# Optimization experiments

Hardware: AMD Instinct MI355X
Metric: run time of the kernel (lower is better)

The kernel has to match this reference:

```python
import jax, jax.numpy as jnp
import numpy as np

D = 1024
H = 16
DK = D // H


def apply_rope(x):
    # x: [B, H, T, dk]; interleaved-pair RoPE as in the torch source
    T, dim = x.shape[-2], x.shape[-1]
    inv_freq = 1.0 / (10000.0 ** (jnp.arange(0, dim, 2, dtype=x.dtype) / dim))  # [dk/2]
    pos = jnp.arange(T, dtype=x.dtype)
    sinusoid = pos[:, None] * inv_freq[None, :]  # [T, dk/2]
    sin, cos = jnp.sin(sinusoid), jnp.cos(sinusoid)
    x1, x2 = x[..., ::2], x[..., 1::2]
    rot = jnp.stack([x1 * cos - x2 * sin, x1 * sin + x2 * cos], axis=-1)
    return rot.reshape(x.shape)


def setup_inputs() -> dict:
    key = jax.random.key(0)
    k1, k2, k3, k4, k5 = jax.random.split(key, 5)
    B, T = 2, 2048
    s = 1.0 / np.sqrt(D)
    return {
        "x": jax.random.normal(k1, (B, T, D), dtype=jnp.float32),
        "W_qkv": jax.random.normal(k2, (D, 3 * D), dtype=jnp.float32) * s,
        "b_qkv": jnp.zeros((3 * D,), dtype=jnp.float32),
        "W_out": jax.random.normal(k3, (D, D), dtype=jnp.float32) * s,
        "b_out": jnp.zeros((D,), dtype=jnp.float32),
    }


def reference(x, W_qkv, b_qkv, W_out, b_out):
    B, T, C = x.shape
    qkv = x @ W_qkv + b_qkv  # [B, T, 3D]
    qkv = qkv.reshape(B, T, 3, H, DK).transpose(2, 0, 3, 1, 4)  # [3, B, H, T, dk]
    q, k, v = qkv[0], qkv[1], qkv[2]
    q, k = apply_rope(q), apply_rope(k)
    scores = jnp.einsum("bhtd,bhsd->bhts", q, k) / jnp.sqrt(jnp.asarray(DK, x.dtype))
    causal = jnp.tril(jnp.ones((T, T), dtype=bool))
    scores = jnp.where(causal, scores, jnp.asarray(-1e9, x.dtype))
    probs = jax.nn.softmax(scores, axis=-1)
    attn = jnp.einsum("bhts,bhsd->bhtd", probs, v)  # [B, H, T, dk]
    out = attn.transpose(0, 2, 1, 3).reshape(B, T, C)  # b h t d -> b t (h d)
    return out @ W_out + b_out
```

## Files before the change

kernel.cpp:

```cpp
#include <hip/hip_runtime.h>
#include <math.h>

#define DMODEL 1024
#define NHEAD  16
#define HDK    64
#define BATCH  2
#define SEQ    2048
#define MROWS  (BATCH*SEQ)
#define NQKV   (3*DMODEL)
#define LOG2_10000 13.287712379549449f
#define INV2PI 0.15915494309189535f
#define SCALE_LOG2E 0.1803368801111137f
#define M_FIX 8.0f

typedef __attribute__((ext_vector_type(8))) short bf16x8;
typedef __attribute__((ext_vector_type(4))) short s16x4;
typedef __attribute__((ext_vector_type(4))) float f32x4;
typedef __attribute__((ext_vector_type(2))) unsigned int u32x2;

__device__ __forceinline__ short f2bf(float f) {
    union { float f; unsigned u; } v; v.f = f;
    unsigned r = v.u + 0x7fffu + ((v.u >> 16) & 1u);
    return (short)(r >> 16);
}

__device__ __forceinline__ float fast_exp2(float x) {
#if __has_builtin(__builtin_amdgcn_exp2f)
    return __builtin_amdgcn_exp2f(x);
#else
    return exp2f(x);
#endif
}

__device__ __forceinline__ void gld_lds16(const short* g, short* l) {
    __builtin_amdgcn_global_load_lds(
        (const __attribute__((address_space(1))) void*)g,
        (__attribute__((address_space(3))) void*)l, 16, 0, 0);
}

__global__ __launch_bounds__(256) void prep_kernel(
    const float* __restrict__ x, const float* __restrict__ wqkv,
    const float* __restrict__ wout,
    short* __restrict__ xb, short* __restrict__ wqkv_t, short* __restrict__ wout_t)
{
    __shared__ short tile[32][33];
    const int tid = threadIdx.x;
    if (blockIdx.x < 2048) {
        const int i = (blockIdx.x * 256 + tid) * 8;
        float4 a = *(const float4*)(x + i);
        float4 b = *(const float4*)(x + i + 4);
        bf16x8 o;
        o[0] = f2bf(a.x); o[1] = f2bf(a.y); o[2] = f2bf(a.z); o[3] = f2bf(a.w);
        o[4] = f2bf(b.x); o[5] = f2bf(b.y); o[6] = f2bf(b.z); o[7] = f2bf(b.w);
        *(bf16x8*)(xb + i) = o;
        return;
    }
    const int bx = blockIdx.x - 2048;
    int nx = bx & 127;
    const int ky = bx >> 7;
    const float* in; short* out; int N;
    if (nx < 96) { in = wqkv; out = wqkv_t; N = NQKV; }
    else         { in = wout; out = wout_t; N = DMODEL; nx -= 96; }
    const int tx = tid & 31, ty = tid >> 5;
    const int n0 = nx * 32, k0 = ky * 32;
    #pragma unroll
    for (int i = 0; i < 32; i += 8)
        tile[ty + i][tx] = f2bf(in[(size_t)(k0 + ty + i) * N + n0 + tx]);
    __syncthreads();
    #pragma unroll
    for (int i = 0; i < 32; i += 8)
        out[(size_t)(n0 + ty + i) * DMODEL + k0 + tx] = tile[tx][ty + i];
}

__global__ __launch_bounds__(256) void qkv_gemm_kernel(
    const short* __restrict__ xb, const short* __restrict__ Wt,
    const float* __restrict__ bias,
    short* __restrict__ qd, short* __restrict__ kd, short* __restrict__ vtb)
{
    __shared__ __align__(16) short As[3][128 * 32];
    __shared__ __align__(16) short Bs[3][128 * 32];
    const int tid = threadIdx.x;
    const int lane = tid & 63, wave = tid >> 6;
    const int wm = wave & 1, wn = wave >> 1;
    const int l15 = lane & 15, quad = lane >> 4;
    const int n0 = blockIdx.x * 128, m0 = blockIdx.y * 128;
    const int srow = lane >> 2, sc = lane & 3;
    const int scp = sc ^ ((srow >> 1) & 3);
    const int rdx = (l15 >> 1) & 3;

    const short* gA1 = xb + (size_t)(m0 + wave * 32 + srow) * DMODEL + scp * 8;
    const short* gA2 = gA1 + (size_t)16 * DMODEL;
    const short* gB1 = Wt + (size_t)(n0 + wave * 32 + srow) * DMODEL + scp * 8;
    const short* gB2 = gB1 + (size_t)16 * DMODEL;
    const int lofsA1 = (wave * 32) * 32;
    const int lofsA2 = (wave * 32 + 16) * 32;

    f32x4 zero = {0.f, 0.f, 0.f, 0.f};
    f32x4 acc[4][4];
    #pragma unroll
    for (int i = 0; i < 4; ++i)
        #pragma unroll
        for (int j = 0; j < 4; ++j) acc[i][j] = zero;

#define QKV_COMPUTE(CUR)                                                          \
    {                                                                             \
        bf16x8 af[4], bfr[4];                                                     \
        _Pragma("unroll")                                                         \
        for (int i = 0; i < 4; ++i)                                               \
            af[i] = *(const bf16x8*)&As[CUR][(wm * 64 + i * 16 + l15) * 32 + (quad ^ rdx) * 8]; \
        _Pragma("unroll")                                                         \
        for (int j = 0; j < 4; ++j)                                               \
            bfr[j] = *(const bf16x8*)&Bs[CUR][(wn * 64 + j * 16 + l15) * 32 + (quad ^ rdx) * 8]; \
        _Pragma("unroll")                                                         \
        for (int i = 0; i < 4; ++i)                                               \
            _Pragma("unroll")                                                     \
            for (int j = 0; j < 4; ++j)                                           \
                acc[i][j] = __builtin_amdgcn_mfma_f32_16x16x32_bf16(af[i], bfr[j], acc[i][j], 0, 0, 0); \
    }

    gld_lds16(gA1, &As[0][lofsA1]);
    gld_lds16(gA2, &As[0][lofsA2]);
    gld_lds16(gB1, &Bs[0][lofsA1]);
    gld_lds16(gB2, &Bs[0][lofsA2]);
    gld_lds16(gA1 + 32, &As[1][lofsA1]);
    gld_lds16(gA2 + 32, &As[1][lofsA2]);
    gld_lds16(gB1 + 32, &Bs[1][lofsA1]);
    gld_lds16(gB2 + 32, &Bs[1][lofsA2]);

    int cur = 0, nx = 2;
    #pragma unroll 3
    for (int k = 0; k < 30; ++k) {
        const int kn = (k + 2) * 32;
        gld_lds16(gA1 + kn, &As[nx][lofsA1]);
        gld_lds16(gA2 + kn, &As[nx][lofsA2]);
        gld_lds16(gB1 + kn, &Bs[nx][lofsA1]);
        gld_lds16(gB2 + kn, &Bs[nx][lofsA2]);
        asm volatile("s_waitcnt vmcnt(8)\n\ts_barrier" ::: "memory");
        QKV_COMPUTE(cur);
        asm volatile("s_barrier" ::: "memory");
        cur = (cur == 2) ? 0 : cur + 1;
        nx  = (nx == 2) ? 0 : nx + 1;
    }
    asm volatile("s_waitcnt vmcnt(4)\n\ts_barrier" ::: "memory");
    QKV_COMPUTE(cur);
    cur = (cur == 2) ? 0 : cur + 1;
    asm volatile("s_waitcnt vmcnt(0)\n\ts_barrier" ::: "memory");
    QKV_COMPUTE(cur);
#undef QKV_COMPUTE

    const int which = n0 >> 10;
    float biasv[4], invf[4];
    int hh[4], dd[4];
    #pragma unroll
    for (int j = 0; j < 4; ++j) {
        const int n = n0 + wn * 64 + j * 16 + l15;
        biasv[j] = bias[n];
        hh[j] = (n & 1023) >> 6;
        dd[j] = n & 63;
        invf[j] = INV2PI * exp2f(-((float)(dd[j] & ~1) / 64.f) * LOG2_10000);
    }
    #pragma unroll
    for (int i = 0; i < 4; ++i) {
        const int mb = m0 + wm * 64 + i * 16 + quad * 4;
        const int b = mb >> 11, tb = mb & (SEQ - 1);
        if (which < 2) {
            #pragma unroll
            for (int j = 0; j < 4; ++j) {
                #pragma unroll
                for (int r = 0; r < 4; ++r) {
                    const int t = tb + r;
                    float val = acc[i][j][r] + biasv[j];
                    const float rev = (float)t * invf[j];
                    const float fr = rev - floorf(rev);
                    const float s = __builtin_amdgcn_sinf(fr);
                    const float c = __builtin_amdgcn_cosf(fr);
                    const float partner = __shfl_xor(val, 1);
                    val = (lane & 1) ? (partner * s + val * c) : (val * c - partner * s);
                    short* dst = (which == 0) ? qd : kd;
                    dst[((size_t)(b * NHEAD + hh[j]) * SEQ + t) * HDK + dd[j]] = f2bf(val);
                }
            }
        } else {
            #pragma unroll
            for (int j = 0; j < 4; ++j) {
                s16x4 sv;
                #pragma unroll
                for (int r = 0; r < 4; ++r)
                    sv[r] = f2bf(acc[i][j][r] + biasv[j]);
                *(s16x4*)&vtb[((size_t)(b * NHEAD + hh[j]) * HDK + dd[j]) * SEQ + tb] = sv;
            }
        }
    }
}

__global__ __launch_bounds__(512) void attn_mfma_kernel(
    const short* __restrict__ qd, const short* __restrict__ kd,
    const short* __restrict__ vt, short* __restrict__ od)
{
    __shared__ __align__(16) short Ks[2][2][64 * 32];
    __shared__ __align__(16) short Vs[2][2][64 * 32];
    __shared__ __align__(16) short Ps[8][16 * 64];
    const int tid = threadIdx.x, lane = tid & 63, w = tid >> 6;
    const int l15 = lane & 15, quad = lane >> 4;
    const int par = w >> 2;
    const int ws = w & 3;
    const int id = (int)blockIdx.x;
    const int c = id & 7, g = id >> 3;
    const int qt = 31 - (g >> 2);
    const int jj = g & 3;
    const int hb = c + 8 * jj;
    const int h = hb & 15, b = hb >> 4;
    const size_t base = ((size_t)(b * NHEAD + h)) * SEQ * HDK;
    const int stid = tid & 255;
    const int hi = tid >> 8;
    const int srow = stid >> 2, sc = stid & 3;
    const int lofs = srow * 32 + (sc ^ ((srow >> 1) & 3)) * 8;
    const int rdx = (l15 >> 1) & 3;
    const int pmask = (l15 & 3) << 2;
    f32x4 zero = {0.f, 0.f, 0.f, 0.f};

    const short* kp = kd + base + (size_t)(hi * 64 + srow) * HDK + sc * 8;
    const short* vp = vt + base + (size_t)srow * SEQ + hi * 64 + sc * 8;

    const int q0 = qt * 64;
    const int trow = q0 + ws * 16 + l15;
    bf16x8 qf[2];
    {
        const short* qrow = qd + base + (size_t)trow * HDK;
        qf[0] = *(const bf16x8*)(qrow + quad * 8);
        qf[1] = *(const bf16x8*)(qrow + 32 + quad * 8);
    }
    float l_acc = 0.f;
    f32x4 o[4];
    #pragma unroll
    for (int j = 0; j < 4; ++j) o[j] = zero;

    const int nkt = qt + 1;
    const int npair = (nkt + 1) >> 1;
    short* myPs = &Ps[w][0];

    bf16x8 rk[2], rv[2];
    rk[0] = *(const bf16x8*)kp; rk[1] = *(const bf16x8*)(kp + 32);
    rv[0] = *(const bf16x8*)vp; rv[1] = *(const bf16x8*)(vp + 32);

    for (int p = 0; p < npair; ++p) {
        __syncthreads();
        *(bf16x8*)&Ks[hi][0][lofs] = rk[0];
        *(bf16x8*)&Ks[hi][1][lofs] = rk[1];
        *(bf16x8*)&Vs[hi][0][lofs] = rv[0];
        *(bf16x8*)&Vs[hi][1][lofs] = rv[1];
        __syncthreads();
        if (p + 1 < npair) {
            const int sn = (2 * p + 2) * 64;
            const short* kn = kp + (size_t)sn * HDK;
            const short* vn = vp + sn;
            rk[0] = *(const bf16x8*)kn; rk[1] = *(const bf16x8*)(kn + 32);
            rv[0] = *(const bf16x8*)vn; rv[1] = *(const bf16x8*)(vn + 32);
        }

        const int kt = 2 * p + par;
        if (kt < nkt) {
            f32x4 sacc[4];
            __builtin_amdgcn_s_setprio(1);
            #pragma unroll
            for (int j = 0; j < 4; ++j) {
                const int ro = (j * 16 + l15) * 32 + (quad ^ rdx) * 8;
                bf16x8 kf0 = *(const bf16x8*)&Ks[par][0][ro];
                bf16x8 kf1 = *(const bf16x8*)&Ks[par][1][ro];
                sacc[j] = __builtin_amdgcn_mfma_f32_16x16x32_bf16(kf0, qf[0], zero, 0, 0, 0);
                sacc[j] = __builtin_amdgcn_mfma_f32_16x16x32_bf16(kf1, qf[1], sacc[j], 0, 0, 0);
            }
            __builtin_amdgcn_s_setprio(0);
            if (kt == nkt - 1) {
                const int s0 = kt * 64;
                #pragma unroll
                for (int j = 0; j < 4; ++j) {
                    float pv[4];
                    #pragma unroll
                    for (int r = 0; r < 4; ++r) {
                        const int scol = s0 + j * 16 + quad * 4 + r;
                        const float sv = sacc[j][r] * SCALE_LOG2E - M_FIX;
                        pv[r] = (scol > trow) ? 0.f : fast_exp2(sv);
                        l_acc += pv[r];
                    }
                    unsigned pk0, pk1;
                    asm("v_cvt_pk_bf16_f32 %0, %1, %2" : "=v"(pk0) : "v"(pv[0]), "v"(pv[1]));
                    asm("v_cvt_pk_bf16_f32 %0, %1, %2" : "=v"(pk1) : "v"(pv[2]), "v"(pv[3]));
                    const int cc = (j * 4 + quad) ^ pmask;
                    u32x2 pkv = {pk0, pk1};
                    *(u32x2*)&myPs[l15 * 64 + cc * 4] = pkv;
                }
            } else {
                #pragma unroll
                for (int j = 0; j < 4; ++j) {
                    float pv[4];
                    #pragma unroll
                    for (int r = 0; r < 4; ++r) {
                        pv[r] = fast_exp2(sacc[j][r] * SCALE_LOG2E - M_FIX);
                        l_acc += pv[r];
                    }
                    unsigned pk0, pk1;
                    asm("v_cvt_pk_bf16_f32 %0, %1, %2" : "=v"(pk0) : "v"(pv[0]), "v"(pv[1]));
                    asm("v_cvt_pk_bf16_f32 %0, %1, %2" : "=v"(pk1) : "v"(pv[2]), "v"(pv[3]));
                    const int cc = (j * 4 + quad) ^ pmask;
                    u32x2 pkv = {pk0, pk1};
                    *(u32x2*)&myPs[l15 * 64 + cc * 4] = pkv;
                }
            }
            bf16x8 pf0 = *(const bf16x8*)&myPs[l15 * 64 + ((quad * 2) ^ pmask) * 4];
            bf16x8 pf1 = *(const bf16x8*)&myPs[l15 * 64 + ((8 + quad * 2) ^ pmask) * 4];
            __builtin_amdgcn_s_setprio(1);
            #pragma unroll
            for (int j = 0; j < 4; ++j) {
                const int ro = (j * 16 + l15) * 32 + (quad ^ rdx) * 8;
                bf16x8 vf0 = *(const bf16x8*)&Vs[par][0][ro];
                bf16x8 vf1 = *(const bf16x8*)&Vs[par][1][ro];
                o[j] = __builtin_amdgcn_mfma_f32_16x16x32_bf16(pf0, vf0, o[j], 0, 0, 0);
                o[j] = __builtin_amdgcn_mfma_f32_16x16x32_bf16(pf1, vf1, o[j], 0, 0, 0);
            }
            __builtin_amdgcn_s_setprio(0);
        }
    }

    float sr = l_acc;
    sr += __shfl_xor(sr, 16);
    sr += __shfl_xor(sr, 32);

    __syncthreads();
    float* ob   = (float*)&Ks[0][0][0];
    float* lbuf = (float*)&Vs[0][0][0];
    lbuf[w * 16 + l15] = sr;
    if (par == 1) {
        const int bi = (ws * 64 + lane) * 16;
        #pragma unroll
        for (int j = 0; j < 4; ++j)
            #pragma unroll
            for (int r = 0; r < 4; ++r) ob[bi + j * 4 + r] = o[j][r];
    }
    __syncthreads();
    if (par == 0) {
        const int bi = (ws * 64 + lane) * 16;
        #pragma unroll
        for (int j = 0; j < 4; ++j)
            #pragma unroll
            for (int r = 0; r < 4; ++r) o[j][r] += ob[bi + j * 4 + r];

        #pragma unroll
        for (int r = 0; r < 4; ++r) {
            const int qq = quad * 4 + r;
            const float lt = lbuf[ws * 16 + qq] + lbuf[(ws + 4) * 16 + qq];
            const float inv = 1.f / lt;
            const int t = q0 + ws * 16 + qq;
            #pragma unroll
            for (int j = 0; j < 4; ++j)
                od[((size_t)(b * SEQ + t) * NHEAD + h) * HDK + j * 16 + l15] =
                    f2bf(o[j][r] * inv);
        }
    }
}

__global__ __launch_bounds__(256) void out_gemm_kernel(
    const short* __restrict__ Ab, const short* __restrict__ Wt,
    const float* __restrict__ bias, float* __restrict__ out)
{
    __shared__ __align__(16) short As[2][128 * 32];
    __shared__ __align__(16) short Bs[2][64 * 32];
    const int tid = threadIdx.x;
    const int lane = tid & 63, wave = tid >> 6;
    const int wm = wave & 1, wn = wave >> 1;
    const int l15 = lane & 15, quad = lane >> 4;
    const int n0 = blockIdx.x * 64, m0 = blockIdx.y * 128;
    const int srow = lane >> 2, sc = lane & 3;
    const int scp = sc ^ ((srow >> 1) & 3);
    const int rdx = (l15 >> 1) & 3;

    const short* gA1 = Ab + (size_t)(m0 + wave * 32 + srow) * DMODEL + scp * 8;
    const short* gA2 = gA1 + (size_t)16 * DMODEL;
    const short* gB1 = Wt + (size_t)(n0 + wave * 16 + srow) * DMODEL + scp * 8;
    const int lofsA1 = (wave * 32) * 32;
    const int lofsA2 = (wave * 32 + 16) * 32;
    const int lofsB  = (wave * 16) * 32;

    f32x4 zero = {0.f, 0.f, 0.f, 0.f};
    f32x4 acc[4][2];
    #pragma unroll
    for (int i = 0; i < 4; ++i)
        #pragma unroll
        for (int j = 0; j < 2; ++j) acc[i][j] = zero;

    gld_lds16(gA1, &As[0][lofsA1]);
    gld_lds16(gA2, &As[0][lofsA2]);
    gld_lds16(gB1, &Bs[0][lofsB]);
    __syncthreads();

    for (int k = 0; k < DMODEL / 32; ++k) {
        const int cur = k & 1;
        if (k + 1 < DMODEL / 32) {
            const int kn = (k + 1) * 32;
            gld_lds16(gA1 + kn, &As[cur ^ 1][lofsA1]);
            gld_lds16(gA2 + kn, &As[cur ^ 1][lofsA2]);
            gld_lds16(gB1 + kn, &Bs[cur ^ 1][lofsB]);
        }
        bf16x8 af[4], bfr[2];
        #pragma unroll
        for (int i = 0; i < 4; ++i)
            af[i] = *(const bf16x8*)&As[cur][(wm * 64 + i * 16 + l15) * 32 + (quad ^ rdx) * 8];
        #pragma unroll
        for (int j = 0; j < 2; ++j)
            bfr[j] = *(const bf16x8*)&Bs[cur][(wn * 32 + j * 16 + l15) * 32 + (quad ^ rdx) * 8];
        #pragma unroll
        for (int i = 0; i < 4; ++i)
            #pragma unroll
            for (int j = 0; j < 2; ++j)
                acc[i][j] = __builtin_amdgcn_mfma_f32_16x16x32_bf16(af[i], bfr[j], acc[i][j], 0, 0, 0);
        __syncthreads();
    }

    #pragma unroll
    for (int j = 0; j < 2; ++j) {
        const int n = n0 + wn * 32 + j * 16 + l15;
        const float bv = bias[n];
        #pragma unroll
        for (int i = 0; i < 4; ++i)
            #pragma unroll
            for (int r = 0; r < 4; ++r) {
                const int m = m0 + wm * 64 + i * 16 + quad * 4 + r;
                out[(size_t)m * DMODEL + n] = acc[i][j][r] + bv;
            }
    }
}

extern "C" void kernel_launch(void* const* d_in, const int* in_sizes, int n_in,
                              void* d_out, int out_size, void* d_ws, size_t ws_size,
                              hipStream_t stream) {
    const float* x    = (const float*)d_in[0];
    const float* Wqkv = (const float*)d_in[1];
    const float* bqkv = (const float*)d_in[2];
    const float* Wout = (const float*)d_in[3];
    const float* bout = (const float*)d_in[4];
    float* out = (float*)d_out;

    short* ws = (short*)d_ws;
    short* xb     = ws;
    short* wqkv_t = xb + (size_t)4 * 1024 * 1024;
    short* wout_t = wqkv_t + (size_t)3 * 1024 * 1024;
    short* qd     = wout_t + (size_t)1024 * 1024;
    short* kd     = qd + (size_t)4 * 1024 * 1024;
    short* vtb    = kd + (size_t)4 * 1024 * 1024;
    short* attn   = vtb + (size_t)4 * 1024 * 1024;

    prep_kernel<<<2048 + 4096, 256, 0, stream>>>(x, Wqkv, Wout, xb, wqkv_t, wout_t);

    qkv_gemm_kernel<<<dim3(NQKV / 128, MROWS / 128), 256, 0, stream>>>(
        xb, wqkv_t, bqkv, qd, kd, vtb);

    attn_mfma_kernel<<<1024, 512, 0, stream>>>(qd, kd, vtb, attn);

    out_gemm_kernel<<<dim3(DMODEL / 64, MROWS / 128), 256, 0, stream>>>(
        attn, wout_t, bout, out);
}
```

Baseline: 186.7 us.

## Stage four KV tiles per barrier in attention and vectorize weight transpose

The attention kernel now loads four 64-key K/V tiles per iteration into shared memory, and each half of the waves processes two tiles back to back. This halves the number of __syncthreads barriers per key sweep and increases the prefetch depth. In exchange it doubles K/V shared memory and prefetch registers, which may lower occupancy. Separately, the prep kernel's weight transpose now uses float4 global loads and 4-wide bf16 stores with a padded tile.

```diff
diff --git a/kernel.cpp b/kernel.cpp
--- a/kernel.cpp
+++ b/kernel.cpp
@@ -43,7 +43,7 @@
     const float* __restrict__ wout,
     short* __restrict__ xb, short* __restrict__ wqkv_t, short* __restrict__ wout_t)
 {
-    __shared__ short tile[32][33];
+    __shared__ __align__(16) short tile[32][36];
     const int tid = threadIdx.x;
     if (blockIdx.x < 2048) {
         const int i = (blockIdx.x * 256 + tid) * 8;
@@ -61,15 +61,21 @@
     const float* in; short* out; int N;
     if (nx < 96) { in = wqkv; out = wqkv_t; N = NQKV; }
     else         { in = wout; out = wout_t; N = DMODEL; nx -= 96; }
-    const int tx = tid & 31, ty = tid >> 5;
     const int n0 = nx * 32, k0 = ky * 32;
-    #pragma unroll
-    for (int i = 0; i < 32; i += 8)
-        tile[ty + i][tx] = f2bf(in[(size_t)(k0 + ty + i) * N + n0 + tx]);
+    {
+        const int kr = tid >> 3, nc4 = tid & 7;
+        float4 v = *(const float4*)&in[(size_t)(k0 + kr) * N + n0 + nc4 * 4];
+        tile[nc4 * 4 + 0][kr] = f2bf(v.x);
+        tile[nc4 * 4 + 1][kr] = f2bf(v.y);
+        tile[nc4 * 4 + 2][kr] = f2bf(v.z);
+        tile[nc4 * 4 + 3][kr] = f2bf(v.w);
+    }
     __syncthreads();
-    #pragma unroll
-    for (int i = 0; i < 32; i += 8)
-        out[(size_t)(n0 + ty + i) * DMODEL + k0 + tx] = tile[tx][ty + i];
+    {
+        const int nr = tid >> 3, kc4 = tid & 7;
+        *(s16x4*)&out[(size_t)(n0 + nr) * DMODEL + k0 + kc4 * 4] =
+            *(const s16x4*)&tile[nr][kc4 * 4];
+    }
 }
 
 __global__ __launch_bounds__(256) void qkv_gemm_kernel(
@@ -197,8 +203,8 @@
     const short* __restrict__ qd, const short* __restrict__ kd,
     const short* __restrict__ vt, short* __restrict__ od)
 {
-    __shared__ __align__(16) short Ks[2][2][64 * 32];
-    __shared__ __align__(16) short Vs[2][2][64 * 32];
+    __shared__ __align__(16) short Ks[4][2][64 * 32];
+    __shared__ __align__(16) short Vs[4][2][64 * 32];
     __shared__ __align__(16) short Ps[8][16 * 64];
     const int tid = threadIdx.x, lane = tid & 63, w = tid >> 6;
     const int l15 = lane & 15, quad = lane >> 4;
@@ -219,8 +225,10 @@
     const int pmask = (l15 & 3) << 2;
     f32x4 zero = {0.f, 0.f, 0.f, 0.f};
 
-    const short* kp = kd + base + (size_t)(hi * 64 + srow) * HDK + sc * 8;
-    const short* vp = vt + base + (size_t)srow * SEQ + hi * 64 + sc * 8;
+    const short* kpA = kd + base + (size_t)(hi * 64 + srow) * HDK + sc * 8;
+    const short* vpA = vt + base + (size_t)srow * SEQ + hi * 64 + sc * 8;
+    const short* kpB = kpA + (size_t)128 * HDK;
+    const short* vpB = vpA + 128;
 
     const int q0 = qt * 64;
     const int trow = q0 + ws * 16 + l15;
@@ -236,37 +244,46 @@
     for (int j = 0; j < 4; ++j) o[j] = zero;
 
     const int nkt = qt + 1;
-    const int npair = (nkt + 1) >> 1;
+    const int nquad = (nkt + 3) >> 2;
     short* myPs = &Ps[w][0];
 
-    bf16x8 rk[2], rv[2];
-    rk[0] = *(const bf16x8*)kp; rk[1] = *(const bf16x8*)(kp + 32);
-    rv[0] = *(const bf16x8*)vp; rv[1] = *(const bf16x8*)(vp + 32);
-
-    for (int p = 0; p < npair; ++p) {
+    bf16x8 rk[2][2], rv[2][2];
+    rk[0][0] = *(const bf16x8*)kpA; rk[0][1] = *(const bf16x8*)(kpA + 32);
+    rk[1][0] = *(const bf16x8*)kpB; rk[1][1] = *(const bf16x8*)(kpB + 32);
+    rv[0][0] = *(const bf16x8*)vpA; rv[0][1] = *(const bf16x8*)(vpA + 32);
+    rv[1][0] = *(const bf16x8*)vpB; rv[1][1] = *(const bf16x8*)(vpB + 32);
+
+    for (int p = 0; p < nquad; ++p) {
         __syncthreads();
-        *(bf16x8*)&Ks[hi][0][lofs] = rk[0];
-        *(bf16x8*)&Ks[hi][1][lofs] = rk[1];
-        *(bf16x8*)&Vs[hi][0][lofs] = rv[0];
-        *(bf16x8*)&Vs[hi][1][lofs] = rv[1];
+        *(bf16x8*)&Ks[hi][0][lofs]     = rk[0][0]; *(bf16x8*)&Ks[hi][1][lofs]     = rk[0][1];
+        *(bf16x8*)&Ks[hi + 2][0][lofs] = rk[1][0]; *(bf16x8*)&Ks[hi + 2][1][lofs] = rk[1][1];
+        *(bf16x8*)&Vs[hi][0][lofs]     = rv[0][0]; *(bf16x8*)&Vs[hi][1][lofs]     = rv[0][1];
+        *(bf16x8*)&Vs[hi + 2][0][lofs] = rv[1][0]; *(bf16x8*)&Vs[hi + 2][1][lofs] = rv[1][1];
         __syncthreads();
-        if (p + 1 < npair) {
-            const int sn = (2 * p + 2) * 64;
-            const short* kn = kp + (size_t)sn * HDK;
-            const short* vn = vp + sn;
-            rk[0] = *(const bf16x8*)kn; rk[1] = *(const bf16x8*)(kn + 32);
-            rv[0] = *(const bf16x8*)vn; rv[1] = *(const bf16x8*)(vn + 32);
+        if (p + 1 < nquad) {
+            const int sn = (4 * p + 4) * 64;
+            const short* knA = kpA + (size_t)sn * HDK;
+            const short* vnA = vpA + sn;
+            const short* knB = knA + (size_t)128 * HDK;
+            const short* vnB = vnA + 128;
+            rk[0][0] = *(const bf16x8*)knA; rk[0][1] = *(const bf16x8*)(knA + 32);
+            rk[1][0] = *(const bf16x8*)knB; rk[1][1] = *(const bf16x8*)(knB + 32);
+            rv[0][0] = *(const bf16x8*)vnA; rv[0][1] = *(const bf16x8*)(vnA + 32);
+            rv[1][0] = *(const bf16x8*)vnB; rv[1][1] = *(const bf16x8*)(vnB + 32);
         }
 
-        const int kt = 2 * p + par;
-        if (kt < nkt) {
+        #pragma unroll
+        for (int u = 0; u < 2; ++u) {
+            const int kt = 4 * p + par * 2 + u;
+            if (kt >= nkt) break;
+            const int ts = par * 2 + u;
             f32x4 sacc[4];
             __builtin_amdgcn_s_setprio(1);
             #pragma unroll
             for (int j = 0; j < 4; ++j) {
                 const int ro = (j * 16 + l15) * 32 + (quad ^ rdx) * 8;
-                bf16x8 kf0 = *(const bf16x8*)&Ks[par][0][ro];
-                bf16x8 kf1 = *(const bf16x8*)&Ks[par][1][ro];
+                bf16x8 kf0 = *(const bf16x8*)&Ks[ts][0][ro];
+                bf16x8 kf1 = *(const bf16x8*)&Ks[ts][1][ro];
                 sacc[j] = __builtin_amdgcn_mfma_f32_16x16x32_bf16(kf0, qf[0], zero, 0, 0, 0);
                 sacc[j] = __builtin_amdgcn_mfma_f32_16x16x32_bf16(kf1, qf[1], sacc[j], 0, 0, 0);
             }
@@ -313,8 +330,8 @@
             #pragma unroll
             for (int j = 0; j < 4; ++j) {
                 const int ro = (j * 16 + l15) * 32 + (quad ^ rdx) * 8;
-                bf16x8 vf0 = *(const bf16x8*)&Vs[par][0][ro];
-                bf16x8 vf1 = *(const bf16x8*)&Vs[par][1][ro];
+                bf16x8 vf0 = *(const bf16x8*)&Vs[ts][0][ro];
+                bf16x8 vf1 = *(const bf16x8*)&Vs[ts][1][ro];
                 o[j] = __builtin_amdgcn_mfma_f32_16x16x32_bf16(pf0, vf0, o[j], 0, 0, 0);
                 o[j] = __builtin_amdgcn_mfma_f32_16x16x32_bf16(pf1, vf1, o[j], 0, 0, 0);
             }
```

Measured after the change: 185.2 us. No clear change (-0.8%).
